# Optimization experiments

Measured on AMD Instinct MI355X. Metric: run time of the kernel, lower is better.

Reference implementation:

```python
import jax, jax.numpy as jnp
import numpy as np

B, T, D, H = 4, 2048, 1024, 16
HD = D // H  # head_dim = 64


def setup_inputs() -> dict:
    key = jax.random.key(0)
    k1, k2, k3 = jax.random.split(key, 3)
    s = 0.02
    return {
        "x": jax.random.normal(k1, (B, T, D), dtype=jnp.float32),
        "qkv_w": jax.random.normal(k2, (D, 3 * D), dtype=jnp.float32) * s,
        "qkv_b": jnp.zeros((3 * D,), dtype=jnp.float32),
        "proj_w": jax.random.normal(k3, (D, D), dtype=jnp.float32) * s,
        "proj_b": jnp.zeros((D,), dtype=jnp.float32),
    }


def reference(x, qkv_w, qkv_b, proj_w, proj_b):
    b, t, d = x.shape
    qkv = x @ qkv_w + qkv_b                       # [B,T,3D]
    q, k, v = jnp.split(qkv, 3, axis=-1)
    # [B,T,D] -> [B,H,T,hd]
    q = q.reshape(b, t, H, HD).transpose(0, 2, 1, 3)
    k = k.reshape(b, t, H, HD).transpose(0, 2, 1, 3)
    v = v.reshape(b, t, H, HD).transpose(0, 2, 1, 3)
    att = jnp.einsum("bhqd,bhkd->bhqk", q, k) / np.sqrt(HD).astype(np.float32)
    causal = jnp.tril(jnp.ones((t, t), dtype=bool))
    att = jnp.where(causal[None, None], att, jnp.finfo(att.dtype).min)
    att = jax.nn.softmax(att, axis=-1)
    out = jnp.einsum("bhqk,bhkd->bhqd", att, v)   # [B,H,T,hd]
    out = out.transpose(0, 2, 1, 3).reshape(b, t, H * HD)
    out = out @ proj_w + proj_b                   # dropout p=0.0 -> identity
    return out
```

## Files before the change

### kernel.cpp

```cpp
#include <hip/hip_runtime.h>
#include <hip/hip_bf16.h>

#define Bsz 4
#define Tsz 2048
#define Dsz 1024
#define Hsz 16
#define HDsz 64

typedef __attribute__((ext_vector_type(8))) __bf16 bf16x8;
typedef __attribute__((ext_vector_type(4))) __bf16 bf16x4;
typedef __attribute__((ext_vector_type(4))) float f32x4;
typedef __attribute__((ext_vector_type(2))) float f32x2;
typedef unsigned short u16;
typedef unsigned int u32;

#define DEVI static __device__ __forceinline__

DEVI u16 f2bf(float f) {
    __bf16 h = (__bf16)f;
    union { __bf16 h; u16 u; } c; c.h = h; return c.u;
}
DEVI bf16x8 ld_bf8(const u16* p) { return *reinterpret_cast<const bf16x8*>(p); }

DEVI void gll16(const u16* g, u16* lds) {
    __builtin_amdgcn_global_load_lds(
        (const __attribute__((address_space(1))) u32*)g,
        (__attribute__((address_space(3))) u32*)lds, 16, 0, 0);
}

DEVI void mfma16(f32x4& c, f32x2 a, f32x2 b) {
    asm("v_mfma_f32_16x16x16_bf16 %0, %1, %2, %0" : "+v"(c) : "v"(a), "v"(b));
}

__global__ __launch_bounds__(256)
void conv_bf16(const float* __restrict__ X, u16* __restrict__ Xb)
{
    const size_t i = ((size_t)blockIdx.x * 256 + threadIdx.x) * 8;
    const float4 a = *(const float4*)(X + i);
    const float4 b = *(const float4*)(X + i + 4);
    u16 h[8] = { f2bf(a.x), f2bf(a.y), f2bf(a.z), f2bf(a.w),
                 f2bf(b.x), f2bf(b.y), f2bf(b.z), f2bf(b.w) };
    *(uint4*)(Xb + i) = *(uint4*)h;
}

__global__ __launch_bounds__(256)
void transpose_w(const float* __restrict__ W, u16* __restrict__ WT, int K, int N)
{
    __shared__ float tile[64][65];
    const int n0 = blockIdx.x * 64, k0 = blockIdx.y * 64;
    const int t = threadIdx.x;
    #pragma unroll
    for (int i = 0; i < 4; ++i) {
        const int idx = i*256 + t;
        const int row = idx >> 4, c4 = (idx & 15) * 4;
        const float4 v = *(const float4*)(W + (size_t)(k0 + row)*N + n0 + c4);
        tile[row][c4+0] = v.x; tile[row][c4+1] = v.y;
        tile[row][c4+2] = v.z; tile[row][c4+3] = v.w;
    }
    __syncthreads();
    #pragma unroll
    for (int j = 0; j < 2; ++j) {
        const int idx = j*256 + t;
        const int nr = idx >> 3, kc = (idx & 7) * 8;
        u16 h[8];
        #pragma unroll
        for (int e = 0; e < 8; ++e) h[e] = f2bf(tile[kc + e][nr]);
        *(uint4*)(WT + (size_t)(n0 + nr)*K + k0 + kc) = *(uint4*)h;
    }
}

template<int EPI>
__global__ __launch_bounds__(256, 4)
void gemm128(const u16* __restrict__ A, const u16* __restrict__ Bt,
             const float* __restrict__ bias, float* __restrict__ Cf,
             u16* __restrict__ Qo, u16* __restrict__ Ko, u16* __restrict__ Vo,
             int M, int N, int K)
{
    __shared__ u16 As[2][128][32];
    __shared__ u16 Bs[2][128][32];
    const int tN = blockIdx.x, tM = blockIdx.y;
    const int t = threadIdx.x, l = t & 63, w = t >> 6;
    const int wm = w >> 1, wn = w & 1;
    const int lrow = l & 15, lk = l >> 4;

    f32x4 acc[4][4] = {};

    const u16* Ag = A  + (size_t)tM * 128 * K;
    const u16* Bg = Bt + (size_t)tN * 128 * K;

    int srow[2], sch[2];
    #pragma unroll
    for (int r = 0; r < 2; ++r) {
        const int c = r*256 + t;
        srow[r] = c >> 2;
        sch[r]  = (c & 3) ^ ((srow[r] >> 1) & 3);
    }
    const size_t ldso = (size_t)(t & 192) * 8;

    #pragma unroll
    for (int r = 0; r < 2; ++r) {
        gll16(Ag + (size_t)srow[r]*K + sch[r]*8, &As[0][0][0] + (size_t)r*2048 + ldso);
        gll16(Bg + (size_t)srow[r]*K + sch[r]*8, &Bs[0][0][0] + (size_t)r*2048 + ldso);
    }
    __syncthreads();

    int cur = 0;
    for (int ks = 0; ks < K; ks += 32) {
        if (ks + 32 < K) {
            const int nb = cur ^ 1;
            #pragma unroll
            for (int r = 0; r < 2; ++r) {
                gll16(Ag + (size_t)srow[r]*K + ks + 32 + sch[r]*8,
                      &As[nb][0][0] + (size_t)r*2048 + ldso);
                gll16(Bg + (size_t)srow[r]*K + ks + 32 + sch[r]*8,
                      &Bs[nb][0][0] + (size_t)r*2048 + ldso);
            }
        }
        bf16x8 a[4], bb[4];
        #pragma unroll
        for (int i = 0; i < 4; ++i) {
            const int ar = wm*64 + i*16 + lrow;
            a[i] = ld_bf8(&As[cur][ar][(lk ^ ((ar >> 1) & 3)) * 8]);
        }
        #pragma unroll
        for (int j = 0; j < 4; ++j) {
            const int br = wn*64 + j*16 + lrow;
            bb[j] = ld_bf8(&Bs[cur][br][(lk ^ ((br >> 1) & 3)) * 8]);
        }
        __builtin_amdgcn_s_setprio(1);
        #pragma unroll
        for (int i = 0; i < 4; ++i)
        #pragma unroll
        for (int j = 0; j < 4; ++j)
            acc[i][j] = __builtin_amdgcn_mfma_f32_16x16x32_bf16(a[i], bb[j], acc[i][j], 0, 0, 0);
        __builtin_amdgcn_s_setprio(0);
        __syncthreads();
        cur ^= 1;
    }

    #pragma unroll
    for (int i = 0; i < 4; ++i)
    #pragma unroll
    for (int j = 0; j < 4; ++j)
    #pragma unroll
    for (int r = 0; r < 4; ++r) {
        const int row = tM*128 + wm*64 + i*16 + lk*4 + r;
        const int col = tN*128 + wn*64 + j*16 + lrow;
        const float v = acc[i][j][r] + bias[col];
        if (EPI == 0) {
            Cf[(size_t)row * N + col] = v;
        } else {
            const int which = col >> 10;
            const int h  = (col & 1023) >> 6;
            const int hd = col & 63;
            const int b  = row >> 11;
            const int tt = row & 2047;
            const int bh = b * Hsz + h;
            const u16 bv = f2bf(v);
            if (which == 0)      Qo[((size_t)bh * Tsz + tt) * HDsz + hd] = bv;
            else if (which == 1) Ko[((size_t)bh * Tsz + tt) * HDsz + hd] = bv;
            else                 Vo[((size_t)bh * HDsz + hd) * Tsz + tt] = bv;
        }
    }
}

__global__ __launch_bounds__(256, 4)
void attn3(const u16* __restrict__ Q, const u16* __restrict__ K,
           const u16* __restrict__ Vt, u16* __restrict__ AO)
{
    __shared__ u16 KV[2][2][64][64];

    const int y = blockIdx.y;
    const int x = blockIdx.x;
    const int idx = (x + (y >> 4)) & 15;
    const int qt = (idx & 1) ? (idx >> 1) : (15 - (idx >> 1));
    const int bh = y;
    const int t = threadIdx.x, w = t >> 6, l = t & 63;
    const int lrow = l & 15, lk = l >> 4;
    const int qw = qt*128 + w*32;
    const int qwmax = qw + 31;
    const int swz = lrow & 7;

    const u16* Qh = Q  + (size_t)bh * Tsz * HDsz;
    const u16* Kh = K  + (size_t)bh * Tsz * HDsz;
    const u16* Vh = Vt + (size_t)bh * HDsz * Tsz;

    bf16x8 qf[2][2];
    #pragma unroll
    for (int f = 0; f < 2; ++f)
    #pragma unroll
    for (int kh = 0; kh < 2; ++kh)
        qf[f][kh] = ld_bf8(&Qh[(size_t)(qw + f*16 + lrow)*HDsz + kh*32 + lk*8]);

    f32x4 o[2][4] = {};
    float m[2] = {-3e38f, -3e38f}, lsum[2] = {0.f, 0.f};

    const int ntile = 2*qt + 2;
    int cur = 0;

    #pragma unroll
    for (int rr = 0; rr < 2; ++rr) {
        const int c = rr*256 + t;
        const int row = c >> 3, gc = (c & 7) ^ (row & 7);
        gll16(Kh + (size_t)row*HDsz + gc*8,
              &KV[0][0][0][0] + (size_t)(rr*256 + (t & 192))*8);
        gll16(Vh + (size_t)row*Tsz + gc*8,
              &KV[0][1][0][0] + (size_t)(rr*256 + (t & 192))*8);
    }
    __syncthreads();

    for (int tk = 0; tk < ntile; ++tk) {
        if (tk + 1 < ntile) {
            const int nkv = (tk + 1) * 64;
            #pragma unroll
            for (int rr = 0; rr < 2; ++rr) {
                const int c = rr*256 + t;
                const int row = c >> 3, gc = (c & 7) ^ (row & 7);
                gll16(Kh + (size_t)(nkv + row)*HDsz + gc*8,
                      &KV[cur^1][0][0][0] + (size_t)(rr*256 + (t & 192))*8);
                gll16(Vh + (size_t)row*Tsz + nkv + gc*8,
                      &KV[cur^1][1][0][0] + (size_t)(rr*256 + (t & 192))*8);
            }
        }
        const int kv0 = tk * 64;
        if (kv0 <= qwmax) {
            const u16 (*Ks)[64] = KV[cur][0];
            const u16 (*Vs)[64] = KV[cur][1];
            const bool fullc    = (kv0 + 63 <= qwmax);
            const bool needmask = (kv0 + 63 > qw);

            f32x4 s[2][4];
            __builtin_amdgcn_s_setprio(1);
            #pragma unroll
            for (int c = 0; c < 4; ++c) {
                if (c >= 2 && !fullc) continue;
                const bf16x8 k0 = ld_bf8(&Ks[c*16 + lrow][((0 + lk) ^ swz) * 8]);
                const bf16x8 k1 = ld_bf8(&Ks[c*16 + lrow][((4 + lk) ^ swz) * 8]);
                #pragma unroll
                for (int f = 0; f < 2; ++f) {
                    f32x4 z = {};
                    z = __builtin_amdgcn_mfma_f32_16x16x32_bf16(k0, qf[f][0], z, 0, 0, 0);
                    z = __builtin_amdgcn_mfma_f32_16x16x32_bf16(k1, qf[f][1], z, 0, 0, 0);
                    s[f][c] = z;
                }
            }
            __builtin_amdgcn_s_setprio(0);

            #pragma unroll
            for (int f = 0; f < 2; ++f) {
                const int q = qw + f*16 + lrow;
                if (needmask) {
                    #pragma unroll
                    for (int c = 0; c < 4; ++c) {
                        if (c >= 2 && !fullc) continue;
                        const int base = kv0 + c*16 + lk*4;
                        #pragma unroll
                        for (int r = 0; r < 4; ++r)
                            if (base + r > q) s[f][c][r] = -1e30f;
                    }
                }
                f32x4 t01;
                #pragma unroll
                for (int r = 0; r < 4; ++r) {
                    t01[r] = fmaxf(s[f][0][r], s[f][1][r]);
                    if (fullc) t01[r] = fmaxf(t01[r], fmaxf(s[f][2][r], s[f][3][r]));
                }
                float mx = fmaxf(fmaxf(t01[0], t01[1]), fmaxf(t01[2], t01[3]));
                mx = fmaxf(mx, __shfl_xor(mx, 16));
                mx = fmaxf(mx, __shfl_xor(mx, 32));
                if (__any(mx > m[f] + 64.f)) {
                    const float mn = fmaxf(m[f], mx);
                    const float al = __expf((m[f] - mn) * 0.125f);
                    lsum[f] *= al;
                    m[f] = mn;
                    #pragma unroll
                    for (int c = 0; c < 4; ++c)
                    #pragma unroll
                    for (int r = 0; r < 4; ++r) o[f][c][r] *= al;
                }
                const float nm8 = -m[f] * 0.125f;
                f32x4 ps4 = {};
                #pragma unroll
                for (int c = 0; c < 4; ++c) {
                    if (c >= 2 && !fullc) continue;
                    #pragma unroll
                    for (int r = 0; r < 4; ++r) {
                        const float p = __expf(fmaf(s[f][c][r], 0.125f, nm8));
                        s[f][c][r] = p;
                        ps4[r] += p;
                    }
                }
                float ps = (ps4[0] + ps4[1]) + (ps4[2] + ps4[3]);
                ps += __shfl_xor(ps, 16);
                ps += __shfl_xor(ps, 32);
                lsum[f] += ps;
            }

            __builtin_amdgcn_s_setprio(1);
            #pragma unroll
            for (int c = 0; c < 4; ++c) {
                if (c >= 2 && !fullc) continue;
                union { bf16x4 v; f32x2 f; } p0, p1;
                #pragma unroll
                for (int r = 0; r < 4; ++r) {
                    p0.v[r] = (__bf16)s[0][c][r];
                    p1.v[r] = (__bf16)s[1][c][r];
                }
                #pragma unroll
                for (int chd = 0; chd < 4; ++chd) {
                    const f32x2 va = *reinterpret_cast<const f32x2*>(
                        &Vs[chd*16 + lrow][(((c*2 + (lk >> 1)) ^ swz) << 3) + ((lk & 1) << 2)]);
                    mfma16(o[0][chd], va, p0.f);
                    mfma16(o[1][chd], va, p1.f);
                }
            }
            __builtin_amdgcn_s_setprio(0);
        }
        __syncthreads();
        cur ^= 1;
    }

    const int b = bh >> 4, h = bh & 15;
    #pragma unroll
    for (int f = 0; f < 2; ++f) {
        const float rl = 1.0f / lsum[f];
        #pragma unroll
        for (int chd = 0; chd < 4; ++chd) {
            u16 ov[4] = { f2bf(o[f][chd][0]*rl), f2bf(o[f][chd][1]*rl),
                          f2bf(o[f][chd][2]*rl), f2bf(o[f][chd][3]*rl) };
            *(ushort4*)(AO + ((size_t)(b*Tsz + qw + f*16 + lrow))*Dsz
                           + h*HDsz + chd*16 + lk*4) = *(ushort4*)ov;
        }
    }
}

extern "C" void kernel_launch(void* const* d_in, const int* in_sizes, int n_in,
                              void* d_out, int out_size, void* d_ws, size_t ws_size,
                              hipStream_t stream)
{
    (void)in_sizes; (void)n_in; (void)out_size; (void)ws_size;

    const float* x      = (const float*)d_in[0];
    const float* qkv_w  = (const float*)d_in[1];
    const float* qkv_b  = (const float*)d_in[2];
    const float* proj_w = (const float*)d_in[3];
    const float* proj_b = (const float*)d_in[4];
    float* out = (float*)d_out;

    char* ws = (char*)d_ws;
    const size_t SZ = (size_t)Bsz * Hsz * Tsz * HDsz * sizeof(u16);
    u16* R0 = (u16*)(ws);
    u16* Qb = (u16*)(ws + SZ);
    u16* Kb = (u16*)(ws + 2*SZ);
    u16* Vt = (u16*)(ws + 3*SZ);
    u16* WQKVT = R0;
    u16* AO    = R0;
    u16* WPT   = Qb;

    u16* Xb = (u16*)d_out;

    const int M = Bsz * Tsz;

    conv_bf16<<<(M*Dsz)/(256*8), 256, 0, stream>>>(x, Xb);
    transpose_w<<<dim3(3*Dsz/64, Dsz/64), 256, 0, stream>>>(qkv_w, WQKVT, Dsz, 3*Dsz);
    gemm128<1><<<dim3(3*Dsz/128, M/128), 256, 0, stream>>>(
        Xb, WQKVT, qkv_b, nullptr, Qb, Kb, Vt, M, 3*Dsz, Dsz);
    attn3<<<dim3(Tsz/128, Bsz*Hsz), 256, 0, stream>>>(Qb, Kb, Vt, AO);
    transpose_w<<<dim3(Dsz/64, Dsz/64), 256, 0, stream>>>(proj_w, WPT, Dsz, Dsz);
    gemm128<0><<<dim3(Dsz/128, M/128), 256, 0, stream>>>(
        AO, WPT, proj_b, out, nullptr, nullptr, nullptr, M, Dsz, Dsz);
}
```

Measured before the change: 215.1 us.

## Triple-buffer GEMM LDS pipeline with one barrier and XCD-aware block remap

The GEMM's double-buffered LDS loop becomes a 3-stage ring: loads run two tiles ahead, and a vmcnt wait plus a single barrier per iteration replace the trailing __syncthreads. The launch grid is flattened to 1D, and block ids are remapped so consecutive tiles land on the same XCD (8-way interleave), aiming for better L2 reuse. LDS per block grows and the launch bound drops from 4 to 3 waves per SIMD. The hand-written vmcnt count assumes a specific number of outstanding loads per stage, so it is fragile if gll16 issues a different count.

Result: faster. 201.6 us (-6.3%).

```diff
diff --git a/kernel.cpp b/kernel.cpp
--- a/kernel.cpp
+++ b/kernel.cpp
@@ -70,15 +70,22 @@
 }
 
 template<int EPI>
-__global__ __launch_bounds__(256, 4)
+__global__ __launch_bounds__(256, 3)
 void gemm128(const u16* __restrict__ A, const u16* __restrict__ Bt,
              const float* __restrict__ bias, float* __restrict__ Cf,
              u16* __restrict__ Qo, u16* __restrict__ Ko, u16* __restrict__ Vo,
              int M, int N, int K)
 {
-    __shared__ u16 As[2][128][32];
-    __shared__ u16 Bs[2][128][32];
-    const int tN = blockIdx.x, tM = blockIdx.y;
+    __shared__ u16 As[3][128][32];
+    __shared__ u16 Bs[3][128][32];
+
+    const int nx  = N >> 7;
+    const int nwg = (int)gridDim.x;
+    const int cpx = nwg >> 3;
+    const int orig = blockIdx.x;
+    const int bid  = (orig & 7) * cpx + (orig >> 3);
+    const int tN = bid % nx, tM = bid / nx;
+
     const int t = threadIdx.x, l = t & 63, w = t >> 6;
     const int wm = w >> 1, wn = w & 1;
     const int lrow = l & 15, lk = l >> 4;
@@ -97,46 +104,55 @@
     }
     const size_t ldso = (size_t)(t & 192) * 8;
 
-    #pragma unroll
-    for (int r = 0; r < 2; ++r) {
-        gll16(Ag + (size_t)srow[r]*K + sch[r]*8, &As[0][0][0] + (size_t)r*2048 + ldso);
-        gll16(Bg + (size_t)srow[r]*K + sch[r]*8, &Bs[0][0][0] + (size_t)r*2048 + ldso);
-    }
-    __syncthreads();
-
+    #define STAGE(buf, ks)                                                      \
+        {                                                                       \
+            _Pragma("unroll")                                                   \
+            for (int r = 0; r < 2; ++r) {                                       \
+                gll16(Ag + (size_t)srow[r]*K + (ks) + sch[r]*8,                 \
+                      &As[buf][0][0] + (size_t)r*2048 + ldso);                  \
+                gll16(Bg + (size_t)srow[r]*K + (ks) + sch[r]*8,                 \
+                      &Bs[buf][0][0] + (size_t)r*2048 + ldso);                  \
+            }                                                                   \
+        }
+
+    STAGE(0, 0);
+    STAGE(1, 32);
+
+    const int nk = K >> 5;
     int cur = 0;
-    for (int ks = 0; ks < K; ks += 32) {
-        if (ks + 32 < K) {
-            const int nb = cur ^ 1;
-            #pragma unroll
-            for (int r = 0; r < 2; ++r) {
-                gll16(Ag + (size_t)srow[r]*K + ks + 32 + sch[r]*8,
-                      &As[nb][0][0] + (size_t)r*2048 + ldso);
-                gll16(Bg + (size_t)srow[r]*K + ks + 32 + sch[r]*8,
-                      &Bs[nb][0][0] + (size_t)r*2048 + ldso);
-            }
-        }
+    for (int i = 0; i < nk; ++i) {
+        asm volatile("s_waitcnt vmcnt(4)" ::: "memory");
+        __builtin_amdgcn_sched_barrier(0);
+        __builtin_amdgcn_s_barrier();
+
         bf16x8 a[4], bb[4];
         #pragma unroll
-        for (int i = 0; i < 4; ++i) {
-            const int ar = wm*64 + i*16 + lrow;
-            a[i] = ld_bf8(&As[cur][ar][(lk ^ ((ar >> 1) & 3)) * 8]);
+        for (int ii = 0; ii < 4; ++ii) {
+            const int ar = wm*64 + ii*16 + lrow;
+            a[ii] = ld_bf8(&As[cur][ar][(lk ^ ((ar >> 1) & 3)) * 8]);
         }
         #pragma unroll
         for (int j = 0; j < 4; ++j) {
             const int br = wn*64 + j*16 + lrow;
             bb[j] = ld_bf8(&Bs[cur][br][(lk ^ ((br >> 1) & 3)) * 8]);
         }
+
+        if (i + 2 < nk) {
+            const int nb = (cur + 2) - ((cur + 2) >= 3 ? 3 : 0);
+            STAGE(nb, (i + 2) * 32);
+        }
+
         __builtin_amdgcn_s_setprio(1);
         #pragma unroll
-        for (int i = 0; i < 4; ++i)
+        for (int ii = 0; ii < 4; ++ii)
         #pragma unroll
         for (int j = 0; j < 4; ++j)
-            acc[i][j] = __builtin_amdgcn_mfma_f32_16x16x32_bf16(a[i], bb[j], acc[i][j], 0, 0, 0);
+            acc[ii][j] = __builtin_amdgcn_mfma_f32_16x16x32_bf16(a[ii], bb[j], acc[ii][j], 0, 0, 0);
         __builtin_amdgcn_s_setprio(0);
-        __syncthreads();
-        cur ^= 1;
-    }
+
+        cur = (cur + 1) - ((cur + 1) >= 3 ? 3 : 0);
+    }
+    #undef STAGE
 
     #pragma unroll
     for (int i = 0; i < 4; ++i)
@@ -363,10 +379,10 @@
 
     conv_bf16<<<(M*Dsz)/(256*8), 256, 0, stream>>>(x, Xb);
     transpose_w<<<dim3(3*Dsz/64, Dsz/64), 256, 0, stream>>>(qkv_w, WQKVT, Dsz, 3*Dsz);
-    gemm128<1><<<dim3(3*Dsz/128, M/128), 256, 0, stream>>>(
+    gemm128<1><<<dim3((3*Dsz/128) * (M/128)), 256, 0, stream>>>(
         Xb, WQKVT, qkv_b, nullptr, Qb, Kb, Vt, M, 3*Dsz, Dsz);
     attn3<<<dim3(Tsz/128, Bsz*Hsz), 256, 0, stream>>>(Qb, Kb, Vt, AO);
     transpose_w<<<dim3(Dsz/64, Dsz/64), 256, 0, stream>>>(proj_w, WPT, Dsz, Dsz);
-    gemm128<0><<<dim3(Dsz/128, M/128), 256, 0, stream>>>(
+    gemm128<0><<<dim3((Dsz/128) * (M/128)), 256, 0, stream>>>(
         AO, WPT, proj_b, out, nullptr, nullptr, nullptr, M, Dsz, Dsz);
 }
```
